# Kernel optimization log

Hardware: AMD Instinct MI355X
Metric: run time of the kernel (lower is better)

The kernel has to match this reference:

```python
import jax, jax.numpy as jnp
import numpy as np

N = 100000
EPS = 1e-16

def gat_conv(x, edge_index, W, a_src, a_dst, bias, heads, out_c):
    # x: [N, F_in]; W: [F_in, heads*out_c]; a_src/a_dst: [heads, out_c]; bias: [heads*out_c]
    n = x.shape[0]
    loops = jnp.arange(n)
    src = jnp.concatenate([edge_index[0], loops])  # add self loops (PyG default)
    dst = jnp.concatenate([edge_index[1], loops])
    h = (x @ W).reshape(n, heads, out_c)                       # [N,H,C]
    s_src = jnp.sum(h * a_src[None], axis=-1)                  # [N,H]
    s_dst = jnp.sum(h * a_dst[None], axis=-1)                  # [N,H]
    e = jax.nn.leaky_relu(s_src[src] + s_dst[dst], 0.2)        # [E,H]
    m = jax.ops.segment_max(e, dst, num_segments=n)            # [N,H]
    ex = jnp.exp(e - m[dst])
    denom = jax.ops.segment_sum(ex, dst, num_segments=n)       # [N,H]
    alpha = ex / (denom[dst] + EPS)                            # [E,H]
    msg = h[src] * alpha[:, :, None]                           # [E,H,C]
    out = jax.ops.segment_sum(msg, dst, num_segments=n)        # [N,H,C]
    return out.reshape(n, heads * out_c) + bias

def setup_inputs() -> dict:
    key = jax.random.key(0)
    ks = jax.random.split(key, 10)
    num_features, num_classes, H = 512, 10, 8
    E = 3200000
    x = jax.random.normal(ks[0], (N, num_features), dtype=jnp.float32)
    edge_index = jax.random.randint(ks[1], (2, E), 0, N, dtype=jnp.int64)
    g = lambda k, shape, fan: jax.random.normal(k, shape, dtype=jnp.float32) * (1.0 / np.sqrt(fan))
    W1 = g(ks[2], (num_features, H * 8), num_features)
    a_src1 = g(ks[3], (H, 8), 8)
    a_dst1 = g(ks[4], (H, 8), 8)
    b1 = jnp.zeros((H * 8,), dtype=jnp.float32)
    W2 = g(ks[5], (H * 8, H * num_classes), H * 8)
    a_src2 = g(ks[6], (H, num_classes), num_classes)
    a_dst2 = g(ks[7], (H, num_classes), num_classes)
    b2 = jnp.zeros((H * num_classes,), dtype=jnp.float32)
    return {"x": x, "edge_index": edge_index, "W1": W1, "a_src1": a_src1,
            "a_dst1": a_dst1, "b1": b1, "W2": W2, "a_src2": a_src2,
            "a_dst2": a_dst2, "b2": b2}

def reference(x, edge_index, W1, a_src1, a_dst1, b1, W2, a_src2, a_dst2, b2):
    # inference mode: dropout = identity
    h = jax.nn.elu(gat_conv(x, edge_index, W1, a_src1, a_dst1, b1, heads=8, out_c=8))
    out = gat_conv(h, edge_index, W2, a_src2, a_dst2, b2, heads=8, out_c=10)
    return jax.nn.log_softmax(out, axis=1)
```

## Files before the change

kernel.cpp:

```cpp
#include <hip/hip_runtime.h>
#include <math.h>

#define NN 100000
#define NE 3200000
#define FIN 512
#define NH 8
#define C1 8
#define HC1 64
#define C2 10
#define HC2 80

#define EPB 4096
#define NBLK 782
#define NBUK 196
#define SCN (NBUK * NBLK)
#define SCNB 150

typedef unsigned int uint;
typedef unsigned short ushort;
using bf16x8 = __attribute__((ext_vector_type(8))) short;
using f32x4  = __attribute__((ext_vector_type(4))) float;

__device__ float g_h1[NN * HC1];
__device__ float g_hact[NN * HC1];
__device__ float g_h2[NN * HC2];
__device__ uint  g_h1b[NN * 32];
__device__ uint  g_h2b[NN * 40];
__device__ uint  g_w1bt[64 * 256];
__device__ float g_ssrc[NN * NH];
__device__ float g_sdst[NN * NH];
__device__ int   g_off8[NBUK * 4096];
__device__ uint  g_pscan[SCN];
__device__ uint  g_bsum2[256];
__device__ uint  g_ebuf[NE];
__device__ int   g_csr[NE];

__device__ __forceinline__ float lrelu(float x) { return fmaxf(x, 0.2f * x); }

__device__ __forceinline__ uint bf16_rne(float x) {
  uint u = __float_as_uint(x);
  u += 0x7fffu + ((u >> 16) & 1u);
  return u >> 16;
}
__device__ __forceinline__ uint packbf2(float lo, float hi) {
  return bf16_rne(lo) | (bf16_rne(hi) << 16);
}
__device__ __forceinline__ float blo(uint v) { return __uint_as_float(v << 16); }
__device__ __forceinline__ float bhi(uint v) { return __uint_as_float(v & 0xffff0000u); }

__global__ __launch_bounds__(256) void p1count_kernel(const int* __restrict__ ei) {
  __shared__ uint cnt[NBUK];
  int tid = threadIdx.x;
  for (int i = tid; i < NBUK; i += 256) cnt[i] = 0;
  __syncthreads();
  const int* dstp = ei + NE;
  int base = blockIdx.x * EPB;
#pragma unroll 4
  for (int k = 0; k < 16; k++) {
    int e = base + k * 256 + tid;
    if (e < NE) atomicAdd(&cnt[dstp[e] >> 9], 1u);
  }
  __syncthreads();
  for (int i = tid; i < NBUK; i += 256) g_pscan[i * NBLK + blockIdx.x] = cnt[i];
}

__global__ __launch_bounds__(1024) void scn_block_kernel() {
  __shared__ uint sd[1024];
  int tid = threadIdx.x;
  int i = blockIdx.x * 1024 + tid;
  uint v = (i < SCN) ? g_pscan[i] : 0;
  sd[tid] = v;
  __syncthreads();
  for (int off = 1; off < 1024; off <<= 1) {
    uint x = (tid >= off) ? sd[tid - off] : 0;
    __syncthreads();
    sd[tid] += x;
    __syncthreads();
  }
  if (i < SCN) g_pscan[i] = sd[tid] - v;
  if (tid == 1023) g_bsum2[blockIdx.x] = sd[1023];
}

__global__ void scn_tops_kernel() {
  __shared__ uint sd[256];
  int tid = threadIdx.x;
  uint v = (tid < SCNB) ? g_bsum2[tid] : 0;
  sd[tid] = v;
  __syncthreads();
  for (int off = 1; off < 256; off <<= 1) {
    uint x = (tid >= off) ? sd[tid - off] : 0;
    __syncthreads();
    sd[tid] += x;
    __syncthreads();
  }
  g_bsum2[tid] = sd[tid] - v;
}

__global__ __launch_bounds__(1024) void scn_add_kernel() {
  int i = blockIdx.x * 1024 + threadIdx.x;
  if (i < SCN) g_pscan[i] += g_bsum2[i >> 10];
}

__global__ __launch_bounds__(256) void p1scatter_kernel(const int* __restrict__ ei) {
  __shared__ uint cur[NBUK];
  int tid = threadIdx.x;
  for (int i = tid; i < NBUK; i += 256) cur[i] = g_pscan[i * NBLK + blockIdx.x];
  __syncthreads();
  const int* srcp = ei;
  const int* dstp = ei + NE;
  int base = blockIdx.x * EPB;
#pragma unroll 4
  for (int k = 0; k < 16; k++) {
    int e = base + k * 256 + tid;
    if (e < NE) {
      int d = dstp[e], s = srcp[e];
      uint pos = atomicAdd(&cur[d >> 9], 1u);
      g_ebuf[pos] = ((uint)(d & 511) << 17) | (uint)s;
    }
  }
}

__global__ __launch_bounds__(1024) void p2build_kernel() {
  __shared__ uint hist[4096];
  __shared__ uint excl[4096];
  __shared__ uint tsum[1024];
  int tid = threadIdx.x;
  int b = blockIdx.x;
  uint bstart = g_pscan[b * NBLK];
  uint bend = (b < NBUK - 1) ? g_pscan[(b + 1) * NBLK] : NE;
  for (int i = tid; i < 4096; i += 1024) hist[i] = 0;
  __syncthreads();
  for (uint j = bstart + tid; j < bend; j += 1024) {
    uint v = g_ebuf[j];
    uint bin = ((v >> 17) << 3) | ((v & 0x1FFFFu) >> 14);
    atomicAdd(&hist[bin], 1u);
  }
  __syncthreads();
  uint h0 = hist[tid * 4 + 0], h1 = hist[tid * 4 + 1];
  uint h2 = hist[tid * 4 + 2], h3 = hist[tid * 4 + 3];
  uint s1 = h0 + h1, s2 = s1 + h2, s3 = s2 + h3;
  tsum[tid] = s3;
  __syncthreads();
  for (int off = 1; off < 1024; off <<= 1) {
    uint x = (tid >= off) ? tsum[tid - off] : 0;
    __syncthreads();
    tsum[tid] += x;
    __syncthreads();
  }
  uint te = tsum[tid] - s3;
  excl[tid * 4 + 0] = te;
  excl[tid * 4 + 1] = te + h0;
  excl[tid * 4 + 2] = te + s1;
  excl[tid * 4 + 3] = te + s2;
  __syncthreads();
  for (int i = tid; i < 4096; i += 1024)
    g_off8[b * 4096 + i] = (int)(bstart + excl[i]);
  for (int i = tid; i < 4096; i += 1024) hist[i] = excl[i];
  __syncthreads();
  for (uint j = bstart + tid; j < bend; j += 1024) {
    uint v = g_ebuf[j];
    uint bin = ((v >> 17) << 3) | ((v & 0x1FFFFu) >> 14);
    uint pos = bstart + atomicAdd(&hist[bin], 1u);
    g_csr[pos] = (int)(v & 0x1FFFFu);
  }
}

__global__ __launch_bounds__(256) void w1cast_kernel(const float* __restrict__ W) {
  int idx = blockIdx.x * 256 + threadIdx.x;
  int n = idx & 63, kp = idx >> 6;
  float lo = W[(2 * kp) * HC1 + n];
  float hi = W[(2 * kp + 1) * HC1 + n];
  g_w1bt[n * 256 + kp] = packbf2(lo, hi);
}

__device__ __forceinline__ int sw_idx(int row, int g) {
  return row * 32 + ((g ^ (row & 7)) << 2);
}

__global__ __launch_bounds__(256) void gemm1_kernel(const float* __restrict__ X) {
  __shared__ uint sA[64 * 32];
  __shared__ uint sB[64 * 32];
  int t = threadIdx.x;
  int w = t >> 6, l = t & 63;
  int q = l >> 4, c = l & 15;
  int r0 = blockIdx.x * 64;
  int sr = t >> 2;
  int sc = t & 3;
  int xrow = r0 + sr; if (xrow >= NN) xrow = NN - 1;
  const float* xbase = &X[(long)xrow * FIN + sc * 16];
  const uint* wbase = &g_w1bt[sr * 256 + sc * 8];
  f32x4 acc[4] = {{0.f,0.f,0.f,0.f},{0.f,0.f,0.f,0.f},{0.f,0.f,0.f,0.f},{0.f,0.f,0.f,0.f}};
  for (int k0 = 0; k0 < FIN; k0 += 64) {
    __syncthreads();
    float4 f0 = *(const float4*)&xbase[k0 + 0];
    float4 f1 = *(const float4*)&xbase[k0 + 4];
    float4 f2 = *(const float4*)&xbase[k0 + 8];
    float4 f3 = *(const float4*)&xbase[k0 + 12];
    uint4 a0 = make_uint4(packbf2(f0.x, f0.y), packbf2(f0.z, f0.w),
                          packbf2(f1.x, f1.y), packbf2(f1.z, f1.w));
    uint4 a1 = make_uint4(packbf2(f2.x, f2.y), packbf2(f2.z, f2.w),
                          packbf2(f3.x, f3.y), packbf2(f3.z, f3.w));
    *(uint4*)&sA[sw_idx(sr, sc * 2 + 0)] = a0;
    *(uint4*)&sA[sw_idx(sr, sc * 2 + 1)] = a1;
    uint4 b0 = *(const uint4*)&wbase[(k0 >> 1) + 0];
    uint4 b1 = *(const uint4*)&wbase[(k0 >> 1) + 4];
    *(uint4*)&sB[sw_idx(sr, sc * 2 + 0)] = b0;
    *(uint4*)&sB[sw_idx(sr, sc * 2 + 1)] = b1;
    __syncthreads();
#pragma unroll
    for (int ks = 0; ks < 2; ks++) {
      int g = ks * 4 + q;
      bf16x8 a = *(const bf16x8*)&sA[sw_idx(w * 16 + c, g)];
#pragma unroll
      for (int nt = 0; nt < 4; nt++) {
        bf16x8 b = *(const bf16x8*)&sB[sw_idx(nt * 16 + c, g)];
        acc[nt] = __builtin_amdgcn_mfma_f32_16x16x32_bf16(a, b, acc[nt], 0, 0, 0);
      }
    }
  }
  int orow0 = r0 + w * 16 + q * 4;
#pragma unroll
  for (int nt = 0; nt < 4; nt++) {
#pragma unroll
    for (int r = 0; r < 4; r++) {
      int row = orow0 + r;
      if (row < NN) g_h1[row * HC1 + nt * 16 + c] = acc[nt][r];
    }
  }
}

template <int LAYER>
__global__ __launch_bounds__(256) void s_kernel(const float* __restrict__ a_src,
                                                const float* __restrict__ a_dst) {
  constexpr int C = (LAYER == 1) ? C1 : C2;
  const float* Hm = (LAYER == 1) ? g_h1 : g_h2;
  uint* Hb = (LAYER == 1) ? g_h1b : g_h2b;
  int t = blockIdx.x * 256 + threadIdx.x;
  if (t >= NN * NH) return;
  int h = t & 7;
  const float* row = &Hm[t * C];
  float ss = 0.f, sdd = 0.f;
  float vals[C];
#pragma unroll
  for (int c = 0; c < C; c++) {
    float v = row[c];
    vals[c] = v;
    ss = fmaf(v, a_src[h * C + c], ss);
    sdd = fmaf(v, a_dst[h * C + c], sdd);
  }
  g_ssrc[t] = ss;
  g_sdst[t] = sdd;
#pragma unroll
  for (int j = 0; j < C / 2; j++)
    Hb[t * (C / 2) + j] = packbf2(vals[2 * j], vals[2 * j + 1]);
}

__global__ __launch_bounds__(256) void agg1_kernel(const float* __restrict__ b1) {
  int wv = __builtin_amdgcn_readfirstlane((int)((blockIdx.x * 256 + threadIdx.x) >> 6));
  int n0 = wv * 8;
  int lane = threadIdx.x & 63;
  int h = lane >> 3;
  int xcd = blockIdx.x & 7;
  const ushort* __restrict__ h1u = (const ushort*)g_h1b;
  float acc[8], wsum[8], sdv[8];
#pragma unroll
  for (int s = 0; s < 8; s++) {
    acc[s] = 0.f;
    wsum[s] = 0.f;
    sdv[s] = g_sdst[(n0 + s) * NH + h];
  }
  for (int rr = 0; rr < 8; rr++) {
    int ra = (rr + xcd) & 7;
#pragma unroll
    for (int s = 0; s < 8; s++) {
      int n = n0 + s;
      int j  = __builtin_amdgcn_readfirstlane(g_off8[n * 8 + ra]);
      int j1 = __builtin_amdgcn_readfirstlane(g_off8[n * 8 + ra + 1]);
      if (j == j1) continue;
      float sd = sdv[s];
      for (; j + 4 <= j1; j += 4) {
        int s0 = __builtin_amdgcn_readfirstlane(g_csr[j + 0]);
        int s1 = __builtin_amdgcn_readfirstlane(g_csr[j + 1]);
        int s2 = __builtin_amdgcn_readfirstlane(g_csr[j + 2]);
        int s3 = __builtin_amdgcn_readfirstlane(g_csr[j + 3]);
        float t0 = g_ssrc[s0 * NH + h];
        float t1 = g_ssrc[s1 * NH + h];
        float t2 = g_ssrc[s2 * NH + h];
        float t3 = g_ssrc[s3 * NH + h];
        uint v0 = h1u[s0 * HC1 + lane];
        uint v1 = h1u[s1 * HC1 + lane];
        uint v2 = h1u[s2 * HC1 + lane];
        uint v3 = h1u[s3 * HC1 + lane];
        float e0 = __expf(lrelu(t0 + sd));
        float e1 = __expf(lrelu(t1 + sd));
        float e2 = __expf(lrelu(t2 + sd));
        float e3 = __expf(lrelu(t3 + sd));
        acc[s] = fmaf(__uint_as_float(v0 << 16), e0, acc[s]);
        acc[s] = fmaf(__uint_as_float(v1 << 16), e1, acc[s]);
        acc[s] = fmaf(__uint_as_float(v2 << 16), e2, acc[s]);
        acc[s] = fmaf(__uint_as_float(v3 << 16), e3, acc[s]);
        wsum[s] += (e0 + e1) + (e2 + e3);
      }
      for (; j < j1; j++) {
        int sx = __builtin_amdgcn_readfirstlane(g_csr[j]);
        float e = __expf(lrelu(g_ssrc[sx * NH + h] + sd));
        acc[s] = fmaf(__uint_as_float((uint)h1u[sx * HC1 + lane] << 16), e, acc[s]);
        wsum[s] += e;
      }
    }
    __syncthreads();
  }
#pragma unroll
  for (int s = 0; s < 8; s++) {
    int n = n0 + s;
    float es = __expf(lrelu(g_ssrc[n * NH + h] + sdv[s]));
    float a = fmaf(g_h1[n * HC1 + lane], es, acc[s]);
    float ws = wsum[s] + es;
    float v = a * (1.f / ws) + b1[lane];
    g_hact[n * HC1 + lane] = v > 0.f ? v : __expf(v) - 1.f;
  }
}

__global__ __launch_bounds__(256) void gemm2_kernel(const float* __restrict__ W) {
  __shared__ float sW[64 * HC2 + 64];
  int tid = threadIdx.x;
  for (int i = tid; i < 64 * HC2; i += 256) sW[i] = W[i];
  for (int i = 64 * HC2 + tid; i < 64 * HC2 + 64; i += 256) sW[i] = 0.f;
  __syncthreads();
  int lane = tid & 63;
  int w0 = (blockIdx.x * 256 + tid) >> 6;
  for (int r = w0; r < NN; r += 8192) {
    float v = g_hact[r * HC1 + lane];
    float acc0 = 0.f, acc1 = 0.f;
#pragma unroll
    for (int k = 0; k < 64; k++) {
      float xk = __shfl(v, k);
      acc0 = fmaf(xk, sW[k * HC2 + lane], acc0);
      acc1 = fmaf(xk, sW[k * HC2 + 64 + lane], acc1);
    }
    g_h2[r * HC2 + lane] = acc0;
    if (lane < 16) g_h2[r * HC2 + 64 + lane] = acc1;
  }
}

__global__ __launch_bounds__(256) void agg2_kernel(float* __restrict__ out,
                                                   const float* __restrict__ b2) {
  int wv = __builtin_amdgcn_readfirstlane((int)((blockIdx.x * 256 + threadIdx.x) >> 6));
  int n0 = wv * 8;
  int lane = threadIdx.x & 63;
  int p = lane < 40 ? lane : 39;
  int h = p / 5;
  int xcd = blockIdx.x & 7;
  float acc0[8], acc1[8], wsum[8], sdv[8];
#pragma unroll
  for (int s = 0; s < 8; s++) {
    acc0[s] = 0.f;
    acc1[s] = 0.f;
    wsum[s] = 0.f;
    sdv[s] = g_sdst[(n0 + s) * NH + h];
  }
  for (int rr = 0; rr < 8; rr++) {
    int ra = (rr + xcd) & 7;
#pragma unroll
    for (int s = 0; s < 8; s++) {
      int n = n0 + s;
      int j  = __builtin_amdgcn_readfirstlane(g_off8[n * 8 + ra]);
      int j1 = __builtin_amdgcn_readfirstlane(g_off8[n * 8 + ra + 1]);
      if (j == j1) continue;
      float sd = sdv[s];
      for (; j + 4 <= j1; j += 4) {
        int s0 = __builtin_amdgcn_readfirstlane(g_csr[j + 0]);
        int s1 = __builtin_amdgcn_readfirstlane(g_csr[j + 1]);
        int s2 = __builtin_amdgcn_readfirstlane(g_csr[j + 2]);
        int s3 = __builtin_amdgcn_readfirstlane(g_csr[j + 3]);
        float t0 = g_ssrc[s0 * NH + h];
        float t1 = g_ssrc[s1 * NH + h];
        float t2 = g_ssrc[s2 * NH + h];
        float t3 = g_ssrc[s3 * NH + h];
        uint v0 = g_h2b[s0 * 40 + p];
        uint v1 = g_h2b[s1 * 40 + p];
        uint v2 = g_h2b[s2 * 40 + p];
        uint v3 = g_h2b[s3 * 40 + p];
        float e0 = __expf(lrelu(t0 + sd));
        float e1 = __expf(lrelu(t1 + sd));
        float e2 = __expf(lrelu(t2 + sd));
        float e3 = __expf(lrelu(t3 + sd));
        acc0[s] = fmaf(blo(v0), e0, acc0[s]); acc1[s] = fmaf(bhi(v0), e0, acc1[s]);
        acc0[s] = fmaf(blo(v1), e1, acc0[s]); acc1[s] = fmaf(bhi(v1), e1, acc1[s]);
        acc0[s] = fmaf(blo(v2), e2, acc0[s]); acc1[s] = fmaf(bhi(v2), e2, acc1[s]);
        acc0[s] = fmaf(blo(v3), e3, acc0[s]); acc1[s] = fmaf(bhi(v3), e3, acc1[s]);
        wsum[s] += (e0 + e1) + (e2 + e3);
      }
      for (; j < j1; j++) {
        int sx = __builtin_amdgcn_readfirstlane(g_csr[j]);
        float e = __expf(lrelu(g_ssrc[sx * NH + h] + sd));
        uint v = g_h2b[sx * 40 + p];
        acc0[s] = fmaf(blo(v), e, acc0[s]); acc1[s] = fmaf(bhi(v), e, acc1[s]);
        wsum[s] += e;
      }
    }
    __syncthreads();
  }
#pragma unroll
  for (int s = 0; s < 8; s++) {
    int n = n0 + s;
    float es = __expf(lrelu(g_ssrc[n * NH + h] + sdv[s]));
    float a0 = fmaf(g_h2[n * HC2 + 2 * p], es, acc0[s]);
    float a1 = fmaf(g_h2[n * HC2 + 2 * p + 1], es, acc1[s]);
    float ws = wsum[s] + es;
    float inv = 1.f / ws;
    float v0 = a0 * inv + b2[2 * p];
    float v1 = a1 * inv + b2[2 * p + 1];
    float mx = fmaxf(v0, v1);
    for (int o = 32; o; o >>= 1) mx = fmaxf(mx, __shfl_xor(mx, o));
    float spart = (lane < 40) ? __expf(v0 - mx) + __expf(v1 - mx) : 0.f;
    for (int o = 32; o; o >>= 1) spart += __shfl_xor(spart, o);
    float lse = mx + __logf(spart);
    if (lane < 40) *(float2*)&out[n * HC2 + 2 * p] = make_float2(v0 - lse, v1 - lse);
  }
}

extern "C" void kernel_launch(void* const* d_in, const int* in_sizes, int n_in,
                              void* d_out, int out_size, void* d_ws, size_t ws_size,
                              hipStream_t stream) {
  (void)in_sizes; (void)n_in; (void)out_size; (void)d_ws; (void)ws_size;
  const float* x   = (const float*)d_in[0];
  const int*   ei  = (const int*)d_in[1];
  const float* W1  = (const float*)d_in[2];
  const float* as1 = (const float*)d_in[3];
  const float* ad1 = (const float*)d_in[4];
  const float* b1  = (const float*)d_in[5];
  const float* W2  = (const float*)d_in[6];
  const float* as2 = (const float*)d_in[7];
  const float* ad2 = (const float*)d_in[8];
  const float* b2  = (const float*)d_in[9];
  float* out = (float*)d_out;

  p1count_kernel<<<NBLK, 256, 0, stream>>>(ei);
  scn_block_kernel<<<SCNB, 1024, 0, stream>>>();
  scn_tops_kernel<<<1, 256, 0, stream>>>();
  scn_add_kernel<<<SCNB, 1024, 0, stream>>>();
  p1scatter_kernel<<<NBLK, 256, 0, stream>>>(ei);
  p2build_kernel<<<NBUK, 1024, 0, stream>>>();

  w1cast_kernel<<<64, 256, 0, stream>>>(W1);
  gemm1_kernel<<<1563, 256, 0, stream>>>(x);
  s_kernel<1><<<3125, 256, 0, stream>>>(as1, ad1);
  agg1_kernel<<<3125, 256, 0, stream>>>(b1);

  gemm2_kernel<<<2048, 256, 0, stream>>>(W2);
  s_kernel<2><<<3125, 256, 0, stream>>>(as2, ad2);
  agg2_kernel<<<3125, 256, 0, stream>>>(out, b2);
}
```

Baseline: 890.8 us.

## Reorder CSR bins source-range-major and stream contiguous edge runs per wave

The CSR build now orders bins by source range first and node second, and keeps the destination-local index packed into each edge word. Each aggregation wave therefore walks one contiguous edge run per source range for 16 nodes instead of 64 tiny per-node segments, which cuts offset loads and loop overhead. Partial sums are flushed to LDS whenever the destination changes, and destination scores are read from LDS. The cost is extra branchy flush logic and LDS traffic, and each wave now covers 16 nodes, so fewer blocks are launched.

```diff
diff --git a/kernel.cpp b/kernel.cpp
--- a/kernel.cpp
+++ b/kernel.cpp
@@ -15,6 +15,7 @@
 #define NBUK 196
 #define SCN (NBUK * NBLK)
 #define SCNB 150
+#define AGGB 1568
 
 typedef unsigned int uint;
 typedef unsigned short ushort;
@@ -29,11 +30,11 @@
 __device__ uint  g_w1bt[64 * 256];
 __device__ float g_ssrc[NN * NH];
 __device__ float g_sdst[NN * NH];
-__device__ int   g_off8[NBUK * 4096];
+__device__ int   g_off8[NBUK * 4096 + 1];
 __device__ uint  g_pscan[SCN];
 __device__ uint  g_bsum2[256];
 __device__ uint  g_ebuf[NE];
-__device__ int   g_csr[NE];
+__device__ uint  g_csr[NE];
 
 __device__ __forceinline__ float lrelu(float x) { return fmaxf(x, 0.2f * x); }
 
@@ -132,7 +133,7 @@
   __syncthreads();
   for (uint j = bstart + tid; j < bend; j += 1024) {
     uint v = g_ebuf[j];
-    uint bin = ((v >> 17) << 3) | ((v & 0x1FFFFu) >> 14);
+    uint bin = (((v & 0x1FFFFu) >> 14) << 9) | (v >> 17);
     atomicAdd(&hist[bin], 1u);
   }
   __syncthreads();
@@ -155,13 +156,14 @@
   __syncthreads();
   for (int i = tid; i < 4096; i += 1024)
     g_off8[b * 4096 + i] = (int)(bstart + excl[i]);
+  if (b == NBUK - 1 && tid == 0) g_off8[NBUK * 4096] = NE;
   for (int i = tid; i < 4096; i += 1024) hist[i] = excl[i];
   __syncthreads();
   for (uint j = bstart + tid; j < bend; j += 1024) {
     uint v = g_ebuf[j];
-    uint bin = ((v >> 17) << 3) | ((v & 0x1FFFFu) >> 14);
+    uint bin = (((v & 0x1FFFFu) >> 14) << 9) | (v >> 17);
     uint pos = bstart + atomicAdd(&hist[bin], 1u);
-    g_csr[pos] = (int)(v & 0x1FFFFu);
+    g_csr[pos] = v;
   }
 }
 
@@ -256,66 +258,97 @@
 }
 
 __global__ __launch_bounds__(256) void agg1_kernel(const float* __restrict__ b1) {
-  int wv = __builtin_amdgcn_readfirstlane((int)((blockIdx.x * 256 + threadIdx.x) >> 6));
-  int n0 = wv * 8;
-  int lane = threadIdx.x & 63;
+  __shared__ float lacc[4][16][64];
+  __shared__ float lw[4][16][8];
+  __shared__ float lsd[4][16][8];
+  int tid = threadIdx.x;
+  int w = tid >> 6, lane = tid & 63;
   int h = lane >> 3;
+  int wv = blockIdx.x * 4 + w;
+  int n0 = wv * 16;
+  int b = n0 >> 9, nl0 = n0 & 511;
+  const ushort* __restrict__ h1u = (const ushort*)g_h1b;
+#pragma unroll
+  for (int s = 0; s < 16; s++) lacc[w][s][lane] = 0.f;
+  for (int k = lane; k < 128; k += 64) {
+    int s = k >> 3, hh = k & 7;
+    int n = n0 + s; if (n >= NN) n = NN - 1;
+    lsd[w][s][hh] = g_sdst[n * NH + hh];
+    lw[w][s][hh] = 0.f;
+  }
   int xcd = blockIdx.x & 7;
-  const ushort* __restrict__ h1u = (const ushort*)g_h1b;
-  float acc[8], wsum[8], sdv[8];
-#pragma unroll
-  for (int s = 0; s < 8; s++) {
-    acc[s] = 0.f;
-    wsum[s] = 0.f;
-    sdv[s] = g_sdst[(n0 + s) * NH + h];
+  int cur = -1;
+  float acc = 0.f, aw = 0.f;
+#define EDGE1(vv, ee, ff)                                    \
+  {                                                          \
+    int nl_ = (int)((vv) >> 17);                             \
+    if (nl_ != cur) {                                        \
+      if (cur >= 0) {                                        \
+        lacc[w][cur - nl0][lane] += acc;                     \
+        if (!(lane & 7)) lw[w][cur - nl0][h] += aw;          \
+      }                                                      \
+      cur = nl_; acc = 0.f; aw = 0.f;                        \
+    }                                                        \
+    acc = fmaf(__uint_as_float((uint)(ff) << 16), (ee), acc);\
+    aw += (ee);                                              \
   }
   for (int rr = 0; rr < 8; rr++) {
     int ra = (rr + xcd) & 7;
-#pragma unroll
-    for (int s = 0; s < 8; s++) {
-      int n = n0 + s;
-      int j  = __builtin_amdgcn_readfirstlane(g_off8[n * 8 + ra]);
-      int j1 = __builtin_amdgcn_readfirstlane(g_off8[n * 8 + ra + 1]);
-      if (j == j1) continue;
-      float sd = sdv[s];
-      for (; j + 4 <= j1; j += 4) {
-        int s0 = __builtin_amdgcn_readfirstlane(g_csr[j + 0]);
-        int s1 = __builtin_amdgcn_readfirstlane(g_csr[j + 1]);
-        int s2 = __builtin_amdgcn_readfirstlane(g_csr[j + 2]);
-        int s3 = __builtin_amdgcn_readfirstlane(g_csr[j + 3]);
-        float t0 = g_ssrc[s0 * NH + h];
-        float t1 = g_ssrc[s1 * NH + h];
-        float t2 = g_ssrc[s2 * NH + h];
-        float t3 = g_ssrc[s3 * NH + h];
-        uint v0 = h1u[s0 * HC1 + lane];
-        uint v1 = h1u[s1 * HC1 + lane];
-        uint v2 = h1u[s2 * HC1 + lane];
-        uint v3 = h1u[s3 * HC1 + lane];
-        float e0 = __expf(lrelu(t0 + sd));
-        float e1 = __expf(lrelu(t1 + sd));
-        float e2 = __expf(lrelu(t2 + sd));
-        float e3 = __expf(lrelu(t3 + sd));
-        acc[s] = fmaf(__uint_as_float(v0 << 16), e0, acc[s]);
-        acc[s] = fmaf(__uint_as_float(v1 << 16), e1, acc[s]);
-        acc[s] = fmaf(__uint_as_float(v2 << 16), e2, acc[s]);
-        acc[s] = fmaf(__uint_as_float(v3 << 16), e3, acc[s]);
-        wsum[s] += (e0 + e1) + (e2 + e3);
-      }
-      for (; j < j1; j++) {
-        int sx = __builtin_amdgcn_readfirstlane(g_csr[j]);
-        float e = __expf(lrelu(g_ssrc[sx * NH + h] + sd));
-        acc[s] = fmaf(__uint_as_float((uint)h1u[sx * HC1 + lane] << 16), e, acc[s]);
-        wsum[s] += e;
-      }
-    }
-    __syncthreads();
-  }
-#pragma unroll
-  for (int s = 0; s < 8; s++) {
+    int idx = b * 4096 + ra * 512 + nl0;
+    int j  = __builtin_amdgcn_readfirstlane(g_off8[idx]);
+    int j1 = __builtin_amdgcn_readfirstlane(g_off8[idx + 16]);
+    for (; j + 4 <= j1; j += 4) {
+      uint v0 = (uint)__builtin_amdgcn_readfirstlane((int)g_csr[j + 0]);
+      uint v1 = (uint)__builtin_amdgcn_readfirstlane((int)g_csr[j + 1]);
+      uint v2 = (uint)__builtin_amdgcn_readfirstlane((int)g_csr[j + 2]);
+      uint v3 = (uint)__builtin_amdgcn_readfirstlane((int)g_csr[j + 3]);
+      int s0 = (int)(v0 & 0x1FFFFu), s1 = (int)(v1 & 0x1FFFFu);
+      int s2 = (int)(v2 & 0x1FFFFu), s3 = (int)(v3 & 0x1FFFFu);
+      float t0 = g_ssrc[s0 * NH + h];
+      float t1 = g_ssrc[s1 * NH + h];
+      float t2 = g_ssrc[s2 * NH + h];
+      float t3 = g_ssrc[s3 * NH + h];
+      uint f0 = h1u[s0 * HC1 + lane];
+      uint f1 = h1u[s1 * HC1 + lane];
+      uint f2 = h1u[s2 * HC1 + lane];
+      uint f3 = h1u[s3 * HC1 + lane];
+      float d0 = lsd[w][(int)(v0 >> 17) - nl0][h];
+      float d1 = lsd[w][(int)(v1 >> 17) - nl0][h];
+      float d2 = lsd[w][(int)(v2 >> 17) - nl0][h];
+      float d3 = lsd[w][(int)(v3 >> 17) - nl0][h];
+      float e0 = __expf(lrelu(t0 + d0));
+      float e1 = __expf(lrelu(t1 + d1));
+      float e2 = __expf(lrelu(t2 + d2));
+      float e3 = __expf(lrelu(t3 + d3));
+      EDGE1(v0, e0, f0);
+      EDGE1(v1, e1, f1);
+      EDGE1(v2, e2, f2);
+      EDGE1(v3, e3, f3);
+    }
+    for (; j < j1; j++) {
+      uint v = (uint)__builtin_amdgcn_readfirstlane((int)g_csr[j]);
+      int sx = (int)(v & 0x1FFFFu);
+      float t = g_ssrc[sx * NH + h];
+      uint f = h1u[sx * HC1 + lane];
+      float d = lsd[w][(int)(v >> 17) - nl0][h];
+      float e = __expf(lrelu(t + d));
+      EDGE1(v, e, f);
+    }
+    __syncthreads();
+  }
+  if (cur >= 0) {
+    lacc[w][cur - nl0][lane] += acc;
+    if (!(lane & 7)) lw[w][cur - nl0][h] += aw;
+  }
+#undef EDGE1
+#pragma unroll
+  for (int s = 0; s < 16; s++) {
     int n = n0 + s;
-    float es = __expf(lrelu(g_ssrc[n * NH + h] + sdv[s]));
-    float a = fmaf(g_h1[n * HC1 + lane], es, acc[s]);
-    float ws = wsum[s] + es;
+    if (n >= NN) break;
+    float sd = lsd[w][s][h];
+    float es = __expf(lrelu(g_ssrc[n * NH + h] + sd));
+    float a = fmaf(g_h1[n * HC1 + lane], es, lacc[w][s][lane]);
+    float ws = lw[w][s][h] + es;
     float v = a * (1.f / ws) + b1[lane];
     g_hact[n * HC1 + lane] = v > 0.f ? v : __expf(v) - 1.f;
   }
@@ -345,72 +378,116 @@
 
 __global__ __launch_bounds__(256) void agg2_kernel(float* __restrict__ out,
                                                    const float* __restrict__ b2) {
-  int wv = __builtin_amdgcn_readfirstlane((int)((blockIdx.x * 256 + threadIdx.x) >> 6));
-  int n0 = wv * 8;
-  int lane = threadIdx.x & 63;
+  __shared__ float lacc[4][16][80];
+  __shared__ float lw[4][16][8];
+  __shared__ float lsd[4][16][8];
+  int tid = threadIdx.x;
+  int w = tid >> 6, lane = tid & 63;
   int p = lane < 40 ? lane : 39;
   int h = p / 5;
+  bool p5 = (lane < 40) && (lane % 5 == 0);
+  int wv = blockIdx.x * 4 + w;
+  int n0 = wv * 16;
+  int b = n0 >> 9, nl0 = n0 & 511;
+#pragma unroll
+  for (int s = 0; s < 16; s++) {
+    if (lane < 40) {
+      lacc[w][s][2 * lane] = 0.f;
+      lacc[w][s][2 * lane + 1] = 0.f;
+    }
+  }
+  for (int k = lane; k < 128; k += 64) {
+    int s = k >> 3, hh = k & 7;
+    int n = n0 + s; if (n >= NN) n = NN - 1;
+    lsd[w][s][hh] = g_sdst[n * NH + hh];
+    lw[w][s][hh] = 0.f;
+  }
   int xcd = blockIdx.x & 7;
-  float acc0[8], acc1[8], wsum[8], sdv[8];
-#pragma unroll
-  for (int s = 0; s < 8; s++) {
-    acc0[s] = 0.f;
-    acc1[s] = 0.f;
-    wsum[s] = 0.f;
-    sdv[s] = g_sdst[(n0 + s) * NH + h];
+  int cur = -1;
+  float a0 = 0.f, a1 = 0.f, aw = 0.f;
+#define EDGE2(vv, ee, ff)                          \
+  {                                                \
+    int nl_ = (int)((vv) >> 17);                   \
+    if (nl_ != cur) {                              \
+      if (cur >= 0) {                              \
+        int ss_ = cur - nl0;                       \
+        if (lane < 40) {                           \
+          lacc[w][ss_][2 * p] += a0;               \
+          lacc[w][ss_][2 * p + 1] += a1;           \
+        }                                          \
+        if (p5) lw[w][ss_][h] += aw;               \
+      }                                            \
+      cur = nl_; a0 = 0.f; a1 = 0.f; aw = 0.f;     \
+    }                                              \
+    a0 = fmaf(blo(ff), (ee), a0);                  \
+    a1 = fmaf(bhi(ff), (ee), a1);                  \
+    aw += (ee);                                    \
   }
   for (int rr = 0; rr < 8; rr++) {
     int ra = (rr + xcd) & 7;
-#pragma unroll
-    for (int s = 0; s < 8; s++) {
-      int n = n0 + s;
-      int j  = __builtin_amdgcn_readfirstlane(g_off8[n * 8 + ra]);
-      int j1 = __builtin_amdgcn_readfirstlane(g_off8[n * 8 + ra + 1]);
-      if (j == j1) continue;
-      float sd = sdv[s];
-      for (; j + 4 <= j1; j += 4) {
-        int s0 = __builtin_amdgcn_readfirstlane(g_csr[j + 0]);
-        int s1 = __builtin_amdgcn_readfirstlane(g_csr[j + 1]);
-        int s2 = __builtin_amdgcn_readfirstlane(g_csr[j + 2]);
-        int s3 = __builtin_amdgcn_readfirstlane(g_csr[j + 3]);
-        float t0 = g_ssrc[s0 * NH + h];
-        float t1 = g_ssrc[s1 * NH + h];
-        float t2 = g_ssrc[s2 * NH + h];
-        float t3 = g_ssrc[s3 * NH + h];
-        uint v0 = g_h2b[s0 * 40 + p];
-        uint v1 = g_h2b[s1 * 40 + p];
-        uint v2 = g_h2b[s2 * 40 + p];
-        uint v3 = g_h2b[s3 * 40 + p];
-        float e0 = __expf(lrelu(t0 + sd));
-        float e1 = __expf(lrelu(t1 + sd));
-        float e2 = __expf(lrelu(t2 + sd));
-        float e3 = __expf(lrelu(t3 + sd));
-        acc0[s] = fmaf(blo(v0), e0, acc0[s]); acc1[s] = fmaf(bhi(v0), e0, acc1[s]);
-        acc0[s] = fmaf(blo(v1), e1, acc0[s]); acc1[s] = fmaf(bhi(v1), e1, acc1[s]);
-        acc0[s] = fmaf(blo(v2), e2, acc0[s]); acc1[s] = fmaf(bhi(v2), e2, acc1[s]);
-        acc0[s] = fmaf(blo(v3), e3, acc0[s]); acc1[s] = fmaf(bhi(v3), e3, acc1[s]);
-        wsum[s] += (e0 + e1) + (e2 + e3);
-      }
-      for (; j < j1; j++) {
-        int sx = __builtin_amdgcn_readfirstlane(g_csr[j]);
-        float e = __expf(lrelu(g_ssrc[sx * NH + h] + sd));
-        uint v = g_h2b[sx * 40 + p];
-        acc0[s] = fmaf(blo(v), e, acc0[s]); acc1[s] = fmaf(bhi(v), e, acc1[s]);
-        wsum[s] += e;
-      }
-    }
-    __syncthreads();
-  }
-#pragma unroll
-  for (int s = 0; s < 8; s++) {
+    int idx = b * 4096 + ra * 512 + nl0;
+    int j  = __builtin_amdgcn_readfirstlane(g_off8[idx]);
+    int j1 = __builtin_amdgcn_readfirstlane(g_off8[idx + 16]);
+    for (; j + 4 <= j1; j += 4) {
+      uint v0 = (uint)__builtin_amdgcn_readfirstlane((int)g_csr[j + 0]);
+      uint v1 = (uint)__builtin_amdgcn_readfirstlane((int)g_csr[j + 1]);
+      uint v2 = (uint)__builtin_amdgcn_readfirstlane((int)g_csr[j + 2]);
+      uint v3 = (uint)__builtin_amdgcn_readfirstlane((int)g_csr[j + 3]);
+      int s0 = (int)(v0 & 0x1FFFFu), s1 = (int)(v1 & 0x1FFFFu);
+      int s2 = (int)(v2 & 0x1FFFFu), s3 = (int)(v3 & 0x1FFFFu);
+      float t0 = g_ssrc[s0 * NH + h];
+      float t1 = g_ssrc[s1 * NH + h];
+      float t2 = g_ssrc[s2 * NH + h];
+      float t3 = g_ssrc[s3 * NH + h];
+      uint f0 = g_h2b[s0 * 40 + p];
+      uint f1 = g_h2b[s1 * 40 + p];
+      uint f2 = g_h2b[s2 * 40 + p];
+      uint f3 = g_h2b[s3 * 40 + p];
+      float d0 = lsd[w][(int)(v0 >> 17) - nl0][h];
+      float d1 = lsd[w][(int)(v1 >> 17) - nl0][h];
+      float d2 = lsd[w][(int)(v2 >> 17) - nl0][h];
+      float d3 = lsd[w][(int)(v3 >> 17) - nl0][h];
+      float e0 = __expf(lrelu(t0 + d0));
+      float e1 = __expf(lrelu(t1 + d1));
+      float e2 = __expf(lrelu(t2 + d2));
+      float e3 = __expf(lrelu(t3 + d3));
+      EDGE2(v0, e0, f0);
+      EDGE2(v1, e1, f1);
+      EDGE2(v2, e2, f2);
+      EDGE2(v3, e3, f3);
+    }
+    for (; j < j1; j++) {
+      uint v = (uint)__builtin_amdgcn_readfirstlane((int)g_csr[j]);
+      int sx = (int)(v & 0x1FFFFu);
+      float t = g_ssrc[sx * NH + h];
+      uint f = g_h2b[sx * 40 + p];
+      float d = lsd[w][(int)(v >> 17) - nl0][h];
+      float e = __expf(lrelu(t + d));
+      EDGE2(v, e, f);
+    }
+    __syncthreads();
+  }
+  if (cur >= 0) {
+    int ss_ = cur - nl0;
+    if (lane < 40) {
+      lacc[w][ss_][2 * p] += a0;
+      lacc[w][ss_][2 * p + 1] += a1;
+    }
+    if (p5) lw[w][ss_][h] += aw;
+  }
+#undef EDGE2
+#pragma unroll
+  for (int s = 0; s < 16; s++) {
     int n = n0 + s;
-    float es = __expf(lrelu(g_ssrc[n * NH + h] + sdv[s]));
-    float a0 = fmaf(g_h2[n * HC2 + 2 * p], es, acc0[s]);
-    float a1 = fmaf(g_h2[n * HC2 + 2 * p + 1], es, acc1[s]);
-    float ws = wsum[s] + es;
+    if (n >= NN) break;
+    float sd = lsd[w][s][h];
+    float es = __expf(lrelu(g_ssrc[n * NH + h] + sd));
+    float x0 = fmaf(g_h2[n * HC2 + 2 * p], es, lacc[w][s][2 * p]);
+    float x1 = fmaf(g_h2[n * HC2 + 2 * p + 1], es, lacc[w][s][2 * p + 1]);
+    float ws = lw[w][s][h] + es;
     float inv = 1.f / ws;
-    float v0 = a0 * inv + b2[2 * p];
-    float v1 = a1 * inv + b2[2 * p + 1];
+    float v0 = x0 * inv + b2[2 * p];
+    float v1 = x1 * inv + b2[2 * p + 1];
     float mx = fmaxf(v0, v1);
     for (int o = 32; o; o >>= 1) mx = fmaxf(mx, __shfl_xor(mx, o));
     float spart = (lane < 40) ? __expf(v0 - mx) + __expf(v1 - mx) : 0.f;
@@ -446,9 +523,9 @@
   w1cast_kernel<<<64, 256, 0, stream>>>(W1);
   gemm1_kernel<<<1563, 256, 0, stream>>>(x);
   s_kernel<1><<<3125, 256, 0, stream>>>(as1, ad1);
-  agg1_kernel<<<3125, 256, 0, stream>>>(b1);
+  agg1_kernel<<<AGGB, 256, 0, stream>>>(b1);
 
   gemm2_kernel<<<2048, 256, 0, stream>>>(W2);
   s_kernel<2><<<3125, 256, 0, stream>>>(as2, ad2);
-  agg2_kernel<<<3125, 256, 0, stream>>>(out, b2);
-}
+  agg2_kernel<<<AGGB, 256, 0, stream>>>(out, b2);
+}
```

After: 924.3 us. 1.04x slower.
